# Optimization experiments

Measured on AMD Instinct MI355X. Metric: run time of the kernel, lower is better.

The kernel has to match this reference:

```python
import jax, jax.numpy as jnp
import numpy as np

N, F, H, C = 50000, 128, 4, 32  # nodes, in-features, heads, per-head dim
E = 800000
D = H * C  # concat output dim = 128


def _tconv(x, src, dst, ea, Wq, bq, Wk, bk, Wv, bv, We, Ws, bs):
    # PyG TransformerConv (concat=True, root_weight=True, beta=False, eval mode)
    n = x.shape[0]
    q = (x @ Wq + bq).reshape(n, H, C)
    k = (x @ Wk + bk).reshape(n, H, C)
    v = (x @ Wv + bv).reshape(n, H, C)
    e = (ea @ We).reshape(-1, H, C)            # edge embedding [E,H,C]
    kj = k[src] + e                            # gathered keys + edge emb
    alpha = jnp.einsum('ehc,ehc->eh', q[dst], kj) / jnp.sqrt(jnp.float32(C))
    amax = jax.ops.segment_max(alpha, dst, num_segments=n)
    ex = jnp.exp(alpha - amax[dst])
    denom = jax.ops.segment_sum(ex, dst, num_segments=n)
    w = ex / (denom[dst] + 1e-16)              # segment softmax over in-edges
    msg = (v[src] + e) * w[:, :, None]
    out = jax.ops.segment_sum(msg, dst, num_segments=n).reshape(n, D)
    return out + x @ Ws + bs                   # skip connection


def setup_inputs() -> dict:
    key = jax.random.key(0)
    ks = jax.random.split(key, 24)
    s = lambda i, shape, scale: jax.random.normal(ks[i], shape, dtype=jnp.float32) * scale
    inp = {
        'x': s(0, (N, F), 1.0),
        'edge_index': jax.random.randint(ks[1], (2, E), 0, N),
        'edge_attr': s(2, (E,), 1.0),
        # layer 1 (in = F)
        'Wq1': s(3, (F, D), 1.0 / np.sqrt(F)), 'bq1': jnp.zeros((D,), jnp.float32),
        'Wk1': s(4, (F, D), 1.0 / np.sqrt(F)), 'bk1': jnp.zeros((D,), jnp.float32),
        'Wv1': s(5, (F, D), 1.0 / np.sqrt(F)), 'bv1': jnp.zeros((D,), jnp.float32),
        'We1': s(6, (1, D), 1.0),
        'Ws1': s(7, (F, D), 1.0 / np.sqrt(F)), 'bs1': jnp.zeros((D,), jnp.float32),
        # layer 2 (in = D)
        'Wq2': s(8, (D, D), 1.0 / np.sqrt(D)), 'bq2': jnp.zeros((D,), jnp.float32),
        'Wk2': s(9, (D, D), 1.0 / np.sqrt(D)), 'bk2': jnp.zeros((D,), jnp.float32),
        'Wv2': s(10, (D, D), 1.0 / np.sqrt(D)), 'bv2': jnp.zeros((D,), jnp.float32),
        'We2': s(11, (1, D), 1.0),
        'Ws2': s(12, (D, D), 1.0 / np.sqrt(D)), 'bs2': jnp.zeros((D,), jnp.float32),
    }
    return inp


def reference(x, edge_index, edge_attr,
              Wq1, bq1, Wk1, bk1, Wv1, bv1, We1, Ws1, bs1,
              Wq2, bq2, Wk2, bk2, Wv2, bv2, We2, Ws2, bs2):
    src, dst = edge_index[0], edge_index[1]
    ea = edge_attr.reshape(-1, 1)
    h = _tconv(x, src, dst, ea, Wq1, bq1, Wk1, bk1, Wv1, bv1, We1, Ws1, bs1)
    h = jax.nn.relu(h)  # dropout is identity in eval mode
    h = _tconv(h, src, dst, ea, Wq2, bq2, Wk2, bk2, Wv2, bv2, We2, Ws2, bs2)
    return jax.nn.relu(h)
```

## Files before the change

### kernel.cpp

```cpp
#include <hip/hip_runtime.h>


#define TPB 256

typedef __attribute__((ext_vector_type(8))) short short8v;
typedef __attribute__((ext_vector_type(8))) unsigned short ushort8v;
typedef __attribute__((ext_vector_type(4))) float f32x4;

__device__ __forceinline__ unsigned short f2bf(float f) {
    unsigned u = __float_as_uint(f);
    u = (u + 0x7FFFu + ((u >> 16) & 1u)) >> 16;
    return (unsigned short)u;
}
__device__ __forceinline__ float bf2f(unsigned short s) {
    return __uint_as_float((unsigned)s << 16);
}
__device__ __forceinline__ float exp2_hw(float x) {
    float r;
    asm("v_exp_f32 %0, %1" : "=v"(r) : "v"(x));
    return r;
}

__global__ void __launch_bounds__(TPB) prepack_k(
    const float* __restrict__ Wq1, const float* __restrict__ Wk1,
    const float* __restrict__ Wv1, const float* __restrict__ Ws1,
    const float* __restrict__ Wq2, const float* __restrict__ Wk2,
    const float* __restrict__ Wv2, const float* __restrict__ Ws2,
    unsigned short* __restrict__ pack)
{
    int i = blockIdx.x * TPB + threadIdx.x;
    int j = i & 7, l = (i >> 3) & 63, t = (i >> 9) & 3, c = (i >> 11) & 7, g = (i >> 14) & 7;
    const float* Wt[8] = {Wq1, Wk1, Wv1, Ws1, Wq2, Wk2, Wv2, Ws2};
    const float* W = Wt[g];
    int kk = t * 32 + (l >> 4) * 8 + j;
    int nn = c * 16 + (l & 15);
    pack[i] = f2bf(W[kk * 128 + nn]);
}

template <bool AF32>
__global__ void __launch_bounds__(TPB) gemm_mfma_k(
    const void* __restrict__ Av, int M,
    const unsigned short* __restrict__ pack,
    const float* __restrict__ bq, const float* __restrict__ bk,
    const float* __restrict__ bv, const float* __restrict__ bs,
    unsigned short* __restrict__ oq, unsigned short* __restrict__ ok,
    unsigned short* __restrict__ ov, float* __restrict__ os)
{
    const int g = blockIdx.y;
    const int row0 = blockIdx.x * 128;
    const int wv = threadIdx.x >> 6;
    const int lane = threadIdx.x & 63;
    const int rbase = row0 + wv * 32;
    const int rlo = lane & 15;
    const int kg = (lane >> 4) * 8;
    const int rof = (lane >> 4) * 4;

    const short8v z8 = {0, 0, 0, 0, 0, 0, 0, 0};
    short8v a[2][4];
#pragma unroll
    for (int m = 0; m < 2; ++m) {
        int row = rbase + m * 16 + rlo;
        if (row >= M) {
#pragma unroll
            for (int t = 0; t < 4; ++t) a[m][t] = z8;
        } else if (AF32) {
            const float* Af = (const float*)Av + (size_t)row * 128 + kg;
#pragma unroll
            for (int t = 0; t < 4; ++t) {
                float4 lo = *(const float4*)(Af + t * 32);
                float4 hi = *(const float4*)(Af + t * 32 + 4);
                short8v p;
                p[0] = (short)f2bf(lo.x); p[1] = (short)f2bf(lo.y);
                p[2] = (short)f2bf(lo.z); p[3] = (short)f2bf(lo.w);
                p[4] = (short)f2bf(hi.x); p[5] = (short)f2bf(hi.y);
                p[6] = (short)f2bf(hi.z); p[7] = (short)f2bf(hi.w);
                a[m][t] = p;
            }
        } else {
            const unsigned short* Ab = (const unsigned short*)Av + (size_t)row * 128 + kg;
#pragma unroll
            for (int t = 0; t < 4; ++t)
                a[m][t] = *(const short8v*)(Ab + t * 32);
        }
    }

    f32x4 acc[2][8];
#pragma unroll
    for (int m = 0; m < 2; ++m)
#pragma unroll
        for (int c = 0; c < 8; ++c)
            acc[m][c] = (f32x4){0.f, 0.f, 0.f, 0.f};

    const unsigned short* bp = pack + (size_t)g * (8 * 4 * 512);
#pragma unroll
    for (int c = 0; c < 8; ++c) {
        short8v b[4];
#pragma unroll
        for (int t = 0; t < 4; ++t)
            b[t] = *(const short8v*)(bp + (c * 4 + t) * 512 + lane * 8);
#pragma unroll
        for (int t = 0; t < 4; ++t) {
            acc[0][c] = __builtin_amdgcn_mfma_f32_16x16x32_bf16(a[0][t], b[t], acc[0][c], 0, 0, 0);
            acc[1][c] = __builtin_amdgcn_mfma_f32_16x16x32_bf16(a[1][t], b[t], acc[1][c], 0, 0, 0);
        }
    }

    const float* bias = g == 0 ? bq : (g == 1 ? bk : (g == 2 ? bv : bs));
    if (g == 3) {
#pragma unroll
        for (int c = 0; c < 8; ++c) {
            float bb = bias[c * 16 + rlo];
#pragma unroll
            for (int m = 0; m < 2; ++m)
#pragma unroll
                for (int j = 0; j < 4; ++j) {
                    int row = rbase + m * 16 + rof + j;
                    if (row < M) os[(size_t)row * 128 + c * 16 + rlo] = acc[m][c][j] + bb;
                }
        }
    } else {
        unsigned short* out = g == 0 ? oq : (g == 1 ? ok : ov);
#pragma unroll
        for (int c = 0; c < 8; ++c) {
            float bb = bias[c * 16 + rlo];
#pragma unroll
            for (int m = 0; m < 2; ++m)
#pragma unroll
                for (int j = 0; j < 4; ++j) {
                    int row = rbase + m * 16 + rof + j;
                    if (row < M) out[(size_t)row * 128 + c * 16 + rlo] = f2bf(acc[m][c][j] + bb);
                }
        }
    }
}

__global__ void __launch_bounds__(TPB) hist_k(const int* __restrict__ dst,
                                              int* __restrict__ deg, int E)
{
    int e = blockIdx.x * TPB + threadIdx.x;
    if (e < E) atomicAdd(&deg[dst[e]], 1);
}

__global__ void __launch_bounds__(TPB) scan_a_k(const int* __restrict__ deg, int n,
                                                int* __restrict__ incl,
                                                int* __restrict__ bsum)
{
    __shared__ int ts[TPB];
    const int base = blockIdx.x * 1024;
    int vals[4], s = 0;
#pragma unroll
    for (int j = 0; j < 4; ++j) {
        int i = base + threadIdx.x * 4 + j;
        vals[j] = (i < n) ? deg[i] : 0;
        s += vals[j];
    }
    ts[threadIdx.x] = s;
    __syncthreads();
    for (int off = 1; off < TPB; off <<= 1) {
        int u = (threadIdx.x >= off) ? ts[threadIdx.x - off] : 0;
        __syncthreads();
        ts[threadIdx.x] += u;
        __syncthreads();
    }
    int run = ts[threadIdx.x] - s;
#pragma unroll
    for (int j = 0; j < 4; ++j) {
        run += vals[j];
        int i = base + threadIdx.x * 4 + j;
        if (i < n) incl[i] = run;
    }
    if (threadIdx.x == TPB - 1) bsum[blockIdx.x] = ts[TPB - 1];
}

__global__ void __launch_bounds__(TPB) scan_b_k(int* __restrict__ bsum, int nb)
{
    __shared__ int ts[TPB];
    int t = threadIdx.x;
    int v = (t < nb) ? bsum[t] : 0;
    ts[t] = v;
    __syncthreads();
    for (int off = 1; off < TPB; off <<= 1) {
        int u = (t >= off) ? ts[t - off] : 0;
        __syncthreads();
        ts[t] += u;
        __syncthreads();
    }
    if (t < nb) bsum[t] = ts[t] - v;
}

__global__ void __launch_bounds__(TPB) finalize_k(const int* __restrict__ incl,
                                                  const int* __restrict__ deg,
                                                  const int* __restrict__ bsum, int n,
                                                  int* __restrict__ row_ptr,
                                                  int* __restrict__ cursor)
{
    const int base = blockIdx.x * 1024;
    const int boff = bsum[blockIdx.x];
#pragma unroll
    for (int j = 0; j < 4; ++j) {
        int i = base + threadIdx.x * 4 + j;
        if (i < n) {
            int iv = incl[i] + boff;
            int st = iv - deg[i];
            row_ptr[i] = st;
            cursor[i] = st;
            if (i == n - 1) row_ptr[n] = iv;
        }
    }
}

__global__ void __launch_bounds__(TPB) scatter_k(
    const int* __restrict__ src, const int* __restrict__ dst,
    const float* __restrict__ ea, int* __restrict__ cursor,
    int2* __restrict__ csr_pair, int E)
{
    int e = blockIdx.x * TPB + threadIdx.x;
    if (e >= E) return;
    int pos = atomicAdd(&cursor[dst[e]], 1);
    csr_pair[pos] = make_int2(src[e], __float_as_int(ea[e]));
}

template <bool BF16OUT>
__global__ void __launch_bounds__(TPB) node_attn_k(
    const unsigned short* __restrict__ q, const unsigned short* __restrict__ k,
    const unsigned short* __restrict__ v, const float* __restrict__ skip,
    const float* __restrict__ We,
    const int* __restrict__ row_ptr, const int2* __restrict__ csr_pair,
    void* __restrict__ outp, int n)
{
    const int node = blockIdx.x * 16 + (threadIdx.x >> 4);
    if (node >= n) return;
    const int l16 = threadIdx.x & 15;
    const int c8 = l16 * 8;

    const float C2 = 0.17677669529663687f * 1.44269504088896f;

    float we8[8], qv[8];
    {
        float4 wlo = *(const float4*)(We + c8);
        float4 whi = *(const float4*)(We + c8 + 4);
        we8[0] = wlo.x; we8[1] = wlo.y; we8[2] = wlo.z; we8[3] = wlo.w;
        we8[4] = whi.x; we8[5] = whi.y; we8[6] = whi.z; we8[7] = whi.w;
        ushort8v qu = *(const ushort8v*)(q + (size_t)node * 128 + c8);
#pragma unroll
        for (int i = 0; i < 8; ++i) qv[i] = bf2f((unsigned short)qu[i]) * C2;
    }

    float qwe = 0.f;
#pragma unroll
    for (int i = 0; i < 8; ++i) qwe = fmaf(qv[i], we8[i], qwe);
    qwe += __shfl_xor(qwe, 1);
    qwe += __shfl_xor(qwe, 2);

    const int p0 = row_ptr[node], p1 = row_ptr[node + 1];

    float m = -3.4e38f, l = 0.f, sae = 0.f;
    float acc[8];
#pragma unroll
    for (int i = 0; i < 8; ++i) acc[i] = 0.f;

    for (int j = p0; j < p1; j += 4) {
        const int last = p1 - 1;
        int2 pr0 = csr_pair[j];
        int2 pr1 = csr_pair[min(j + 1, last)];
        int2 pr2 = csr_pair[min(j + 2, last)];
        int2 pr3 = csr_pair[min(j + 3, last)];
        ushort8v ku0 = *(const ushort8v*)(k + (unsigned)pr0.x * 128u + c8);
        ushort8v ku1 = *(const ushort8v*)(k + (unsigned)pr1.x * 128u + c8);
        ushort8v ku2 = *(const ushort8v*)(k + (unsigned)pr2.x * 128u + c8);
        ushort8v ku3 = *(const ushort8v*)(k + (unsigned)pr3.x * 128u + c8);
        ushort8v vu0 = *(const ushort8v*)(v + (unsigned)pr0.x * 128u + c8);
        ushort8v vu1 = *(const ushort8v*)(v + (unsigned)pr1.x * 128u + c8);
        ushort8v vu2 = *(const ushort8v*)(v + (unsigned)pr2.x * 128u + c8);
        ushort8v vu3 = *(const ushort8v*)(v + (unsigned)pr3.x * 128u + c8);

        float d0 = 0.f, d1 = 0.f, d2 = 0.f, d3 = 0.f;
#pragma unroll
        for (int i = 0; i < 8; ++i) {
            d0 = fmaf(bf2f((unsigned short)ku0[i]), qv[i], d0);
            d1 = fmaf(bf2f((unsigned short)ku1[i]), qv[i], d1);
            d2 = fmaf(bf2f((unsigned short)ku2[i]), qv[i], d2);
            d3 = fmaf(bf2f((unsigned short)ku3[i]), qv[i], d3);
        }
        d0 += __shfl_xor(d0, 1); d0 += __shfl_xor(d0, 2);
        d1 += __shfl_xor(d1, 1); d1 += __shfl_xor(d1, 2);
        d2 += __shfl_xor(d2, 1); d2 += __shfl_xor(d2, 2);
        d3 += __shfl_xor(d3, 1); d3 += __shfl_xor(d3, 2);

        float ea0 = __int_as_float(pr0.y), ea1 = __int_as_float(pr1.y);
        float ea2 = __int_as_float(pr2.y), ea3 = __int_as_float(pr3.y);
        float al0 = fmaf(ea0, qwe, d0);
        float al1 = (j + 1 < p1) ? fmaf(ea1, qwe, d1) : -3.4e38f;
        float al2 = (j + 2 < p1) ? fmaf(ea2, qwe, d2) : -3.4e38f;
        float al3 = (j + 3 < p1) ? fmaf(ea3, qwe, d3) : -3.4e38f;

        float mn = fmaxf(m, fmaxf(fmaxf(al0, al1), fmaxf(al2, al3)));
        float sc = exp2_hw(m - mn);
        float pe0 = exp2_hw(al0 - mn), pe1 = exp2_hw(al1 - mn);
        float pe2 = exp2_hw(al2 - mn), pe3 = exp2_hw(al3 - mn);

        l = fmaf(l, sc, (pe0 + pe1) + (pe2 + pe3));
        sae = fmaf(sae, sc, fmaf(pe3, ea3, fmaf(pe2, ea2, fmaf(pe1, ea1, pe0 * ea0))));
#pragma unroll
        for (int i = 0; i < 8; ++i) {
            float mv = fmaf(pe0, bf2f((unsigned short)vu0[i]),
                       fmaf(pe1, bf2f((unsigned short)vu1[i]),
                       fmaf(pe2, bf2f((unsigned short)vu2[i]),
                            pe3 * bf2f((unsigned short)vu3[i]))));
            acc[i] = fmaf(acc[i], sc, mv);
        }
        m = mn;
    }

    float inv = 1.f / (l + 1e-16f);
    float4 sklo = *(const float4*)(skip + (size_t)node * 128 + c8);
    float4 skhi = *(const float4*)(skip + (size_t)node * 128 + c8 + 4);
    float sk[8] = {sklo.x, sklo.y, sklo.z, sklo.w, skhi.x, skhi.y, skhi.z, skhi.w};
    float o[8];
#pragma unroll
    for (int i = 0; i < 8; ++i)
        o[i] = fmaxf(fmaf(fmaf(sae, we8[i], acc[i]), inv, sk[i]), 0.f);

    if (BF16OUT) {
        ushort8v ov;
#pragma unroll
        for (int i = 0; i < 8; ++i) ov[i] = f2bf(o[i]);
        *(ushort8v*)((unsigned short*)outp + (size_t)node * 128 + c8) = ov;
    } else {
        float* op = (float*)outp + (size_t)node * 128 + c8;
        *(float4*)op = make_float4(o[0], o[1], o[2], o[3]);
        *(float4*)(op + 4) = make_float4(o[4], o[5], o[6], o[7]);
    }
}

extern "C" void kernel_launch(void* const* d_in, const int* in_sizes, int n_in,
                              void* d_out, int out_size, void* d_ws, size_t ws_size,
                              hipStream_t stream)
{
    const float* x   = (const float*)d_in[0];
    const int*   ei  = (const int*)d_in[1];
    const float* ea  = (const float*)d_in[2];
    const float* Wq1 = (const float*)d_in[3];  const float* bq1 = (const float*)d_in[4];
    const float* Wk1 = (const float*)d_in[5];  const float* bk1 = (const float*)d_in[6];
    const float* Wv1 = (const float*)d_in[7];  const float* bv1 = (const float*)d_in[8];
    const float* We1 = (const float*)d_in[9];
    const float* Ws1 = (const float*)d_in[10]; const float* bs1 = (const float*)d_in[11];
    const float* Wq2 = (const float*)d_in[12]; const float* bq2 = (const float*)d_in[13];
    const float* Wk2 = (const float*)d_in[14]; const float* bk2 = (const float*)d_in[15];
    const float* Wv2 = (const float*)d_in[16]; const float* bv2 = (const float*)d_in[17];
    const float* We2 = (const float*)d_in[18];
    const float* Ws2 = (const float*)d_in[19]; const float* bs2 = (const float*)d_in[20];

    const int N = in_sizes[0] / 128;
    const int E = in_sizes[1] / 2;
    const int* src = ei;
    const int* dst = ei + E;
    float* outf = (float*)d_out;

    unsigned short* q  = (unsigned short*)d_ws;
    unsigned short* k  = q + (size_t)N * 128;
    unsigned short* v  = k + (size_t)N * 128;
    float*          s  = (float*)(v + (size_t)N * 128);
    unsigned short* xb = (unsigned short*)(s + (size_t)N * 128);
    unsigned short* pk = xb + (size_t)N * 128;
    int*   row_ptr = (int*)(pk + 131072);
    int*   deg     = row_ptr + (N + 1);
    int*   incl    = deg + N;
    int*   cursor  = incl + N;
    int*   bsum    = cursor + N;
    int2*  csr_pair = (int2*)(((uintptr_t)(bsum + 256) + 7) & ~(uintptr_t)7);

    const int gE   = (E + TPB - 1) / TPB;
    const int nb   = (N + 1023) / 1024;
    const int gN16 = (N + 15) / 16;
    const int gG   = (N + 127) / 128;
    const dim3 gGd(gG, 4);

    hipMemsetAsync(deg, 0, (size_t)N * sizeof(int), stream);
    hist_k<<<gE, TPB, 0, stream>>>(dst, deg, E);
    scan_a_k<<<nb, TPB, 0, stream>>>(deg, N, incl, bsum);
    scan_b_k<<<1, TPB, 0, stream>>>(bsum, nb);
    finalize_k<<<nb, TPB, 0, stream>>>(incl, deg, bsum, N, row_ptr, cursor);
    scatter_k<<<gE, TPB, 0, stream>>>(src, dst, ea, cursor, csr_pair, E);

    prepack_k<<<131072 / TPB, TPB, 0, stream>>>(Wq1, Wk1, Wv1, Ws1,
                                                Wq2, Wk2, Wv2, Ws2, pk);

    gemm_mfma_k<true><<<gGd, TPB, 0, stream>>>(x, N, pk, bq1, bk1, bv1, bs1,
                                               q, k, v, s);
    node_attn_k<true><<<gN16, TPB, 0, stream>>>(q, k, v, s, We1, row_ptr, csr_pair,
                                                xb, N);
    gemm_mfma_k<false><<<gGd, TPB, 0, stream>>>(xb, N, pk + 65536, bq2, bk2, bv2, bs2,
                                                q, k, v, s);
    node_attn_k<false><<<gN16, TPB, 0, stream>>>(q, k, v, s, We2, row_ptr, csr_pair,
                                                 outf, N);
}
```

Before: 312.8 us.

## Software-pipeline neighbor gathers in attention and pre-convert input to bf16

The attention kernel now double-buffers its edge loop: while one batch of four edges is being processed, it issues the CSR pair loads and the K/V row gathers for the following batches, so memory latency overlaps with compute. Separately, the fp32 input is converted to bf16 once by a new kernel, so the first GEMM no longer converts x in each of its four column-group blocks and reads half the bytes. In exchange the attention kernel holds more registers for the two stages, which may lower occupancy, and there is one extra launch plus an extra pass over x.

```diff
diff --git a/kernel.cpp b/kernel.cpp
--- a/kernel.cpp
+++ b/kernel.cpp
@@ -19,6 +19,18 @@
     float r;
     asm("v_exp_f32 %0, %1" : "=v"(r) : "v"(x));
     return r;
+}
+
+__global__ void __launch_bounds__(TPB) cvt_bf16_k(const float* __restrict__ in,
+                                                  unsigned short* __restrict__ out,
+                                                  int n4)
+{
+    int i = blockIdx.x * TPB + threadIdx.x;
+    if (i >= n4) return;
+    float4 v = *(const float4*)(in + (size_t)i * 4);
+    ushort4 o;
+    o.x = f2bf(v.x); o.y = f2bf(v.y); o.z = f2bf(v.z); o.w = f2bf(v.w);
+    *(ushort4*)(out + (size_t)i * 4) = o;
 }
 
 __global__ void __launch_bounds__(TPB) prepack_k(
@@ -37,9 +49,8 @@
     pack[i] = f2bf(W[kk * 128 + nn]);
 }
 
-template <bool AF32>
 __global__ void __launch_bounds__(TPB) gemm_mfma_k(
-    const void* __restrict__ Av, int M,
+    const unsigned short* __restrict__ A, int M,
     const unsigned short* __restrict__ pack,
     const float* __restrict__ bq, const float* __restrict__ bk,
     const float* __restrict__ bv, const float* __restrict__ bs,
@@ -60,28 +71,10 @@
 #pragma unroll
     for (int m = 0; m < 2; ++m) {
         int row = rbase + m * 16 + rlo;
-        if (row >= M) {
-#pragma unroll
-            for (int t = 0; t < 4; ++t) a[m][t] = z8;
-        } else if (AF32) {
-            const float* Af = (const float*)Av + (size_t)row * 128 + kg;
-#pragma unroll
-            for (int t = 0; t < 4; ++t) {
-                float4 lo = *(const float4*)(Af + t * 32);
-                float4 hi = *(const float4*)(Af + t * 32 + 4);
-                short8v p;
-                p[0] = (short)f2bf(lo.x); p[1] = (short)f2bf(lo.y);
-                p[2] = (short)f2bf(lo.z); p[3] = (short)f2bf(lo.w);
-                p[4] = (short)f2bf(hi.x); p[5] = (short)f2bf(hi.y);
-                p[6] = (short)f2bf(hi.z); p[7] = (short)f2bf(hi.w);
-                a[m][t] = p;
-            }
-        } else {
-            const unsigned short* Ab = (const unsigned short*)Av + (size_t)row * 128 + kg;
-#pragma unroll
-            for (int t = 0; t < 4; ++t)
-                a[m][t] = *(const short8v*)(Ab + t * 32);
-        }
+#pragma unroll
+        for (int t = 0; t < 4; ++t)
+            a[m][t] = (row < M) ? *(const short8v*)(A + (size_t)row * 128 + t * 32 + kg)
+                                : z8;
     }
 
     f32x4 acc[2][8];
@@ -220,6 +213,65 @@
     csr_pair[pos] = make_int2(src[e], __float_as_int(ea[e]));
 }
 
+struct Stage {
+    int2 p[4];
+    ushort8v ku[4], vu[4];
+};
+
+__device__ __forceinline__ void attn_step(
+    Stage& cur, Stage& nxt, int j, int p1, int last,
+    const int2* __restrict__ csr_pair,
+    const unsigned short* __restrict__ k, const unsigned short* __restrict__ v,
+    int c8, const float* qv, float qwe,
+    float& m, float& l, float& sae, float* acc)
+{
+    float ea0 = __int_as_float(cur.p[0].y), ea1 = __int_as_float(cur.p[1].y);
+    float ea2 = __int_as_float(cur.p[2].y), ea3 = __int_as_float(cur.p[3].y);
+#pragma unroll
+    for (int t = 0; t < 4; ++t) cur.p[t] = csr_pair[min(j + 8 + t, last)];
+
+#pragma unroll
+    for (int t = 0; t < 4; ++t) {
+        nxt.ku[t] = *(const ushort8v*)(k + (unsigned)nxt.p[t].x * 128u + c8);
+        nxt.vu[t] = *(const ushort8v*)(v + (unsigned)nxt.p[t].x * 128u + c8);
+    }
+
+    float d0 = 0.f, d1 = 0.f, d2 = 0.f, d3 = 0.f;
+#pragma unroll
+    for (int i = 0; i < 8; ++i) {
+        d0 = fmaf(bf2f((unsigned short)cur.ku[0][i]), qv[i], d0);
+        d1 = fmaf(bf2f((unsigned short)cur.ku[1][i]), qv[i], d1);
+        d2 = fmaf(bf2f((unsigned short)cur.ku[2][i]), qv[i], d2);
+        d3 = fmaf(bf2f((unsigned short)cur.ku[3][i]), qv[i], d3);
+    }
+    d0 += __shfl_xor(d0, 1); d0 += __shfl_xor(d0, 2);
+    d1 += __shfl_xor(d1, 1); d1 += __shfl_xor(d1, 2);
+    d2 += __shfl_xor(d2, 1); d2 += __shfl_xor(d2, 2);
+    d3 += __shfl_xor(d3, 1); d3 += __shfl_xor(d3, 2);
+
+    float al0 = fmaf(ea0, qwe, d0);
+    float al1 = (j + 1 < p1) ? fmaf(ea1, qwe, d1) : -3.4e38f;
+    float al2 = (j + 2 < p1) ? fmaf(ea2, qwe, d2) : -3.4e38f;
+    float al3 = (j + 3 < p1) ? fmaf(ea3, qwe, d3) : -3.4e38f;
+
+    float mn = fmaxf(m, fmaxf(fmaxf(al0, al1), fmaxf(al2, al3)));
+    float sc = exp2_hw(m - mn);
+    float pe0 = exp2_hw(al0 - mn), pe1 = exp2_hw(al1 - mn);
+    float pe2 = exp2_hw(al2 - mn), pe3 = exp2_hw(al3 - mn);
+
+    l = fmaf(l, sc, (pe0 + pe1) + (pe2 + pe3));
+    sae = fmaf(sae, sc, fmaf(pe3, ea3, fmaf(pe2, ea2, fmaf(pe1, ea1, pe0 * ea0))));
+#pragma unroll
+    for (int i = 0; i < 8; ++i) {
+        float mv = fmaf(pe0, bf2f((unsigned short)cur.vu[0][i]),
+                   fmaf(pe1, bf2f((unsigned short)cur.vu[1][i]),
+                   fmaf(pe2, bf2f((unsigned short)cur.vu[2][i]),
+                        pe3 * bf2f((unsigned short)cur.vu[3][i]))));
+        acc[i] = fmaf(acc[i], sc, mv);
+    }
+    m = mn;
+}
+
 template <bool BF16OUT>
 __global__ void __launch_bounds__(TPB) node_attn_k(
     const unsigned short* __restrict__ q, const unsigned short* __restrict__ k,
@@ -235,22 +287,19 @@
 
     const float C2 = 0.17677669529663687f * 1.44269504088896f;
 
-    float we8[8], qv[8];
+    float qv[8];
+    float qwe;
     {
         float4 wlo = *(const float4*)(We + c8);
         float4 whi = *(const float4*)(We + c8 + 4);
-        we8[0] = wlo.x; we8[1] = wlo.y; we8[2] = wlo.z; we8[3] = wlo.w;
-        we8[4] = whi.x; we8[5] = whi.y; we8[6] = whi.z; we8[7] = whi.w;
         ushort8v qu = *(const ushort8v*)(q + (size_t)node * 128 + c8);
 #pragma unroll
         for (int i = 0; i < 8; ++i) qv[i] = bf2f((unsigned short)qu[i]) * C2;
-    }
-
-    float qwe = 0.f;
-#pragma unroll
-    for (int i = 0; i < 8; ++i) qwe = fmaf(qv[i], we8[i], qwe);
-    qwe += __shfl_xor(qwe, 1);
-    qwe += __shfl_xor(qwe, 2);
+        qwe = qv[0] * wlo.x + qv[1] * wlo.y + qv[2] * wlo.z + qv[3] * wlo.w +
+              qv[4] * whi.x + qv[5] * whi.y + qv[6] * whi.z + qv[7] * whi.w;
+        qwe += __shfl_xor(qwe, 1);
+        qwe += __shfl_xor(qwe, 2);
+    }
 
     const int p0 = row_ptr[node], p1 = row_ptr[node + 1];
 
@@ -259,60 +308,31 @@
 #pragma unroll
     for (int i = 0; i < 8; ++i) acc[i] = 0.f;
 
-    for (int j = p0; j < p1; j += 4) {
+    if (p0 < p1) {
         const int last = p1 - 1;
-        int2 pr0 = csr_pair[j];
-        int2 pr1 = csr_pair[min(j + 1, last)];
-        int2 pr2 = csr_pair[min(j + 2, last)];
-        int2 pr3 = csr_pair[min(j + 3, last)];
-        ushort8v ku0 = *(const ushort8v*)(k + (unsigned)pr0.x * 128u + c8);
-        ushort8v ku1 = *(const ushort8v*)(k + (unsigned)pr1.x * 128u + c8);
-        ushort8v ku2 = *(const ushort8v*)(k + (unsigned)pr2.x * 128u + c8);
-        ushort8v ku3 = *(const ushort8v*)(k + (unsigned)pr3.x * 128u + c8);
-        ushort8v vu0 = *(const ushort8v*)(v + (unsigned)pr0.x * 128u + c8);
-        ushort8v vu1 = *(const ushort8v*)(v + (unsigned)pr1.x * 128u + c8);
-        ushort8v vu2 = *(const ushort8v*)(v + (unsigned)pr2.x * 128u + c8);
-        ushort8v vu3 = *(const ushort8v*)(v + (unsigned)pr3.x * 128u + c8);
-
-        float d0 = 0.f, d1 = 0.f, d2 = 0.f, d3 = 0.f;
-#pragma unroll
-        for (int i = 0; i < 8; ++i) {
-            d0 = fmaf(bf2f((unsigned short)ku0[i]), qv[i], d0);
-            d1 = fmaf(bf2f((unsigned short)ku1[i]), qv[i], d1);
-            d2 = fmaf(bf2f((unsigned short)ku2[i]), qv[i], d2);
-            d3 = fmaf(bf2f((unsigned short)ku3[i]), qv[i], d3);
-        }
-        d0 += __shfl_xor(d0, 1); d0 += __shfl_xor(d0, 2);
-        d1 += __shfl_xor(d1, 1); d1 += __shfl_xor(d1, 2);
-        d2 += __shfl_xor(d2, 1); d2 += __shfl_xor(d2, 2);
-        d3 += __shfl_xor(d3, 1); d3 += __shfl_xor(d3, 2);
-
-        float ea0 = __int_as_float(pr0.y), ea1 = __int_as_float(pr1.y);
-        float ea2 = __int_as_float(pr2.y), ea3 = __int_as_float(pr3.y);
-        float al0 = fmaf(ea0, qwe, d0);
-        float al1 = (j + 1 < p1) ? fmaf(ea1, qwe, d1) : -3.4e38f;
-        float al2 = (j + 2 < p1) ? fmaf(ea2, qwe, d2) : -3.4e38f;
-        float al3 = (j + 3 < p1) ? fmaf(ea3, qwe, d3) : -3.4e38f;
-
-        float mn = fmaxf(m, fmaxf(fmaxf(al0, al1), fmaxf(al2, al3)));
-        float sc = exp2_hw(m - mn);
-        float pe0 = exp2_hw(al0 - mn), pe1 = exp2_hw(al1 - mn);
-        float pe2 = exp2_hw(al2 - mn), pe3 = exp2_hw(al3 - mn);
-
-        l = fmaf(l, sc, (pe0 + pe1) + (pe2 + pe3));
-        sae = fmaf(sae, sc, fmaf(pe3, ea3, fmaf(pe2, ea2, fmaf(pe1, ea1, pe0 * ea0))));
-#pragma unroll
-        for (int i = 0; i < 8; ++i) {
-            float mv = fmaf(pe0, bf2f((unsigned short)vu0[i]),
-                       fmaf(pe1, bf2f((unsigned short)vu1[i]),
-                       fmaf(pe2, bf2f((unsigned short)vu2[i]),
-                            pe3 * bf2f((unsigned short)vu3[i]))));
-            acc[i] = fmaf(acc[i], sc, mv);
-        }
-        m = mn;
+        Stage A, B;
+#pragma unroll
+        for (int t = 0; t < 4; ++t) A.p[t] = csr_pair[min(p0 + t, last)];
+#pragma unroll
+        for (int t = 0; t < 4; ++t) B.p[t] = csr_pair[min(p0 + 4 + t, last)];
+#pragma unroll
+        for (int t = 0; t < 4; ++t) {
+            A.ku[t] = *(const ushort8v*)(k + (unsigned)A.p[t].x * 128u + c8);
+            A.vu[t] = *(const ushort8v*)(v + (unsigned)A.p[t].x * 128u + c8);
+        }
+        int j = p0;
+        for (;;) {
+            attn_step(A, B, j, p1, last, csr_pair, k, v, c8, qv, qwe, m, l, sae, acc);
+            j += 4; if (j >= p1) break;
+            attn_step(B, A, j, p1, last, csr_pair, k, v, c8, qv, qwe, m, l, sae, acc);
+            j += 4; if (j >= p1) break;
+        }
     }
 
     float inv = 1.f / (l + 1e-16f);
+    float4 wlo = *(const float4*)(We + c8);
+    float4 whi = *(const float4*)(We + c8 + 4);
+    float we8[8] = {wlo.x, wlo.y, wlo.z, wlo.w, whi.x, whi.y, whi.z, whi.w};
     float4 sklo = *(const float4*)(skip + (size_t)node * 128 + c8);
     float4 skhi = *(const float4*)(skip + (size_t)node * 128 + c8 + 4);
     float sk[8] = {sklo.x, sklo.y, sklo.z, sklo.w, skhi.x, skhi.y, skhi.z, skhi.w};
@@ -373,6 +393,7 @@
     const int gE   = (E + TPB - 1) / TPB;
     const int nb   = (N + 1023) / 1024;
     const int gN16 = (N + 15) / 16;
+    const int gCv  = (N * 128 / 4 + TPB - 1) / TPB;
     const int gG   = (N + 127) / 128;
     const dim3 gGd(gG, 4);
 
@@ -385,13 +406,13 @@
 
     prepack_k<<<131072 / TPB, TPB, 0, stream>>>(Wq1, Wk1, Wv1, Ws1,
                                                 Wq2, Wk2, Wv2, Ws2, pk);
-
-    gemm_mfma_k<true><<<gGd, TPB, 0, stream>>>(x, N, pk, bq1, bk1, bv1, bs1,
-                                               q, k, v, s);
+    cvt_bf16_k<<<gCv, TPB, 0, stream>>>(x, xb, N * 128 / 4);
+
+    gemm_mfma_k<<<gGd, TPB, 0, stream>>>(xb, N, pk, bq1, bk1, bv1, bs1, q, k, v, s);
     node_attn_k<true><<<gN16, TPB, 0, stream>>>(q, k, v, s, We1, row_ptr, csr_pair,
                                                 xb, N);
-    gemm_mfma_k<false><<<gGd, TPB, 0, stream>>>(xb, N, pk + 65536, bq2, bk2, bv2, bs2,
-                                                q, k, v, s);
+    gemm_mfma_k<<<gGd, TPB, 0, stream>>>(xb, N, pk + 65536, bq2, bk2, bv2, bs2,
+                                         q, k, v, s);
     node_attn_k<false><<<gN16, TPB, 0, stream>>>(q, k, v, s, We2, row_ptr, csr_pair,
                                                  outf, N);
 }
```

Result: no change. 311.3 us (-0.5%).

## Interleave K and V rows, switch GEMM to 32x32 MFMA, pre-convert x to bf16

Applied to the files above, without the earlier changes.

K and V projections are now stored interleaved in a single buffer with 256-element rows, so each gathered source node's key and value sit next to each other in memory. The GEMM moves from 16x16x32 to 32x32x16 bf16 MFMA tiles, and the weight prepack layout changes to match. Layer-1 input x is converted to bf16 by an extra section of the prepack kernel, which removes the templated fp32 A-load path from the GEMM. The gather is meant to get better locality, at the cost of an extra pass over x and a different accumulator and register footprint in the GEMM.

```diff
diff --git a/kernel.cpp b/kernel.cpp
--- a/kernel.cpp
+++ b/kernel.cpp
@@ -5,7 +5,7 @@
 
 typedef __attribute__((ext_vector_type(8))) short short8v;
 typedef __attribute__((ext_vector_type(8))) unsigned short ushort8v;
-typedef __attribute__((ext_vector_type(4))) float f32x4;
+typedef __attribute__((ext_vector_type(16))) float f32x16;
 
 __device__ __forceinline__ unsigned short f2bf(float f) {
     unsigned u = __float_as_uint(f);
@@ -21,115 +21,101 @@
     return r;
 }
 
-__global__ void __launch_bounds__(TPB) prepack_k(
+__global__ void __launch_bounds__(TPB) prep_cvt_k(
     const float* __restrict__ Wq1, const float* __restrict__ Wk1,
     const float* __restrict__ Wv1, const float* __restrict__ Ws1,
     const float* __restrict__ Wq2, const float* __restrict__ Wk2,
     const float* __restrict__ Wv2, const float* __restrict__ Ws2,
-    unsigned short* __restrict__ pack)
-{
-    int i = blockIdx.x * TPB + threadIdx.x;
-    int j = i & 7, l = (i >> 3) & 63, t = (i >> 9) & 3, c = (i >> 11) & 7, g = (i >> 14) & 7;
-    const float* Wt[8] = {Wq1, Wk1, Wv1, Ws1, Wq2, Wk2, Wv2, Ws2};
-    const float* W = Wt[g];
-    int kk = t * 32 + (l >> 4) * 8 + j;
-    int nn = c * 16 + (l & 15);
-    pack[i] = f2bf(W[kk * 128 + nn]);
-}
-
-template <bool AF32>
+    unsigned short* __restrict__ pack,
+    const float* __restrict__ x, unsigned short* __restrict__ xb, int n4)
+{
+    if (blockIdx.x < 512) {
+        int i = blockIdx.x * TPB + threadIdx.x;
+        int j = i & 7, lane = (i >> 3) & 63, t = (i >> 9) & 7, nc = (i >> 12) & 3, g = (i >> 14) & 7;
+        const float* Wt[8] = {Wq1, Wk1, Wv1, Ws1, Wq2, Wk2, Wv2, Ws2};
+        const float* W = Wt[g];
+        int kk = t * 16 + (lane >> 5) * 8 + j;
+        int nn = nc * 32 + (lane & 31);
+        pack[i] = f2bf(W[kk * 128 + nn]);
+    } else {
+        int i = (blockIdx.x - 512) * TPB + threadIdx.x;
+        if (i >= n4) return;
+        float4 v = *(const float4*)(x + (size_t)i * 4);
+        ushort4 o;
+        o.x = f2bf(v.x); o.y = f2bf(v.y); o.z = f2bf(v.z); o.w = f2bf(v.w);
+        *(ushort4*)(xb + (size_t)i * 4) = o;
+    }
+}
+
 __global__ void __launch_bounds__(TPB) gemm_mfma_k(
-    const void* __restrict__ Av, int M,
+    const unsigned short* __restrict__ A, int M,
     const unsigned short* __restrict__ pack,
     const float* __restrict__ bq, const float* __restrict__ bk,
     const float* __restrict__ bv, const float* __restrict__ bs,
-    unsigned short* __restrict__ oq, unsigned short* __restrict__ ok,
-    unsigned short* __restrict__ ov, float* __restrict__ os)
+    unsigned short* __restrict__ oq, unsigned short* __restrict__ okv,
+    float* __restrict__ os)
 {
     const int g = blockIdx.y;
     const int row0 = blockIdx.x * 128;
     const int wv = threadIdx.x >> 6;
     const int lane = threadIdx.x & 63;
     const int rbase = row0 + wv * 32;
-    const int rlo = lane & 15;
-    const int kg = (lane >> 4) * 8;
-    const int rof = (lane >> 4) * 4;
+    const int arow = rbase + (lane & 31);
+    const int kh = (lane >> 5) * 8;
 
     const short8v z8 = {0, 0, 0, 0, 0, 0, 0, 0};
-    short8v a[2][4];
-#pragma unroll
-    for (int m = 0; m < 2; ++m) {
-        int row = rbase + m * 16 + rlo;
-        if (row >= M) {
-#pragma unroll
-            for (int t = 0; t < 4; ++t) a[m][t] = z8;
-        } else if (AF32) {
-            const float* Af = (const float*)Av + (size_t)row * 128 + kg;
-#pragma unroll
-            for (int t = 0; t < 4; ++t) {
-                float4 lo = *(const float4*)(Af + t * 32);
-                float4 hi = *(const float4*)(Af + t * 32 + 4);
-                short8v p;
-                p[0] = (short)f2bf(lo.x); p[1] = (short)f2bf(lo.y);
-                p[2] = (short)f2bf(lo.z); p[3] = (short)f2bf(lo.w);
-                p[4] = (short)f2bf(hi.x); p[5] = (short)f2bf(hi.y);
-                p[6] = (short)f2bf(hi.z); p[7] = (short)f2bf(hi.w);
-                a[m][t] = p;
+    short8v a[8];
+    if (arow < M) {
+        const unsigned short* Ap = A + (size_t)arow * 128 + kh;
+#pragma unroll
+        for (int t = 0; t < 8; ++t) a[t] = *(const short8v*)(Ap + t * 16);
+    } else {
+#pragma unroll
+        for (int t = 0; t < 8; ++t) a[t] = z8;
+    }
+
+    f32x16 acc[4];
+#pragma unroll
+    for (int nc = 0; nc < 4; ++nc)
+#pragma unroll
+        for (int r = 0; r < 16; ++r) acc[nc][r] = 0.f;
+
+    const unsigned short* bp = pack + (size_t)g * 16384;
+#pragma unroll
+    for (int nc = 0; nc < 4; ++nc) {
+#pragma unroll
+        for (int t = 0; t < 8; ++t) {
+            short8v b = *(const short8v*)(bp + (nc * 8 + t) * 512 + lane * 8);
+            acc[nc] = __builtin_amdgcn_mfma_f32_32x32x16_bf16(a[t], b, acc[nc], 0, 0, 0);
+        }
+    }
+
+    const float* bias = g == 0 ? bq : (g == 1 ? bk : (g == 2 ? bv : bs));
+    const int col = lane & 31;
+    const int rb2 = rbase + 4 * (lane >> 5);
+    if (g == 3) {
+#pragma unroll
+        for (int nc = 0; nc < 4; ++nc) {
+            float bb = bias[nc * 32 + col];
+#pragma unroll
+            for (int r = 0; r < 16; ++r) {
+                int row = rb2 + (r & 3) + 8 * (r >> 2);
+                if (row < M) os[(size_t)row * 128 + nc * 32 + col] = acc[nc][r] + bb;
             }
-        } else {
-            const unsigned short* Ab = (const unsigned short*)Av + (size_t)row * 128 + kg;
-#pragma unroll
-            for (int t = 0; t < 4; ++t)
-                a[m][t] = *(const short8v*)(Ab + t * 32);
-        }
-    }
-
-    f32x4 acc[2][8];
-#pragma unroll
-    for (int m = 0; m < 2; ++m)
-#pragma unroll
-        for (int c = 0; c < 8; ++c)
-            acc[m][c] = (f32x4){0.f, 0.f, 0.f, 0.f};
-
-    const unsigned short* bp = pack + (size_t)g * (8 * 4 * 512);
-#pragma unroll
-    for (int c = 0; c < 8; ++c) {
-        short8v b[4];
-#pragma unroll
-        for (int t = 0; t < 4; ++t)
-            b[t] = *(const short8v*)(bp + (c * 4 + t) * 512 + lane * 8);
-#pragma unroll
-        for (int t = 0; t < 4; ++t) {
-            acc[0][c] = __builtin_amdgcn_mfma_f32_16x16x32_bf16(a[0][t], b[t], acc[0][c], 0, 0, 0);
-            acc[1][c] = __builtin_amdgcn_mfma_f32_16x16x32_bf16(a[1][t], b[t], acc[1][c], 0, 0, 0);
-        }
-    }
-
-    const float* bias = g == 0 ? bq : (g == 1 ? bk : (g == 2 ? bv : bs));
-    if (g == 3) {
-#pragma unroll
-        for (int c = 0; c < 8; ++c) {
-            float bb = bias[c * 16 + rlo];
-#pragma unroll
-            for (int m = 0; m < 2; ++m)
-#pragma unroll
-                for (int j = 0; j < 4; ++j) {
-                    int row = rbase + m * 16 + rof + j;
-                    if (row < M) os[(size_t)row * 128 + c * 16 + rlo] = acc[m][c][j] + bb;
-                }
         }
     } else {
-        unsigned short* out = g == 0 ? oq : (g == 1 ? ok : ov);
-#pragma unroll
-        for (int c = 0; c < 8; ++c) {
-            float bb = bias[c * 16 + rlo];
-#pragma unroll
-            for (int m = 0; m < 2; ++m)
-#pragma unroll
-                for (int j = 0; j < 4; ++j) {
-                    int row = rbase + m * 16 + rof + j;
-                    if (row < M) out[(size_t)row * 128 + c * 16 + rlo] = f2bf(acc[m][c][j] + bb);
-                }
+        unsigned short* out = g == 0 ? oq : okv;
+        const int stride = g == 0 ? 128 : 256;
+        const int goff = g == 2 ? 128 : 0;
+#pragma unroll
+        for (int nc = 0; nc < 4; ++nc) {
+            float bb = bias[nc * 32 + col];
+#pragma unroll
+            for (int r = 0; r < 16; ++r) {
+                int row = rb2 + (r & 3) + 8 * (r >> 2);
+                if (row < M)
+                    out[(size_t)row * stride + goff + nc * 32 + col] = f2bf(acc[nc][r] + bb);
+            }
         }
     }
 }
@@ -222,9 +208,8 @@
 
 template <bool BF16OUT>
 __global__ void __launch_bounds__(TPB) node_attn_k(
-    const unsigned short* __restrict__ q, const unsigned short* __restrict__ k,
-    const unsigned short* __restrict__ v, const float* __restrict__ skip,
-    const float* __restrict__ We,
+    const unsigned short* __restrict__ q, const unsigned short* __restrict__ kv,
+    const float* __restrict__ skip, const float* __restrict__ We,
     const int* __restrict__ row_ptr, const int2* __restrict__ csr_pair,
     void* __restrict__ outp, int n)
 {
@@ -265,14 +250,18 @@
         int2 pr1 = csr_pair[min(j + 1, last)];
         int2 pr2 = csr_pair[min(j + 2, last)];
         int2 pr3 = csr_pair[min(j + 3, last)];
-        ushort8v ku0 = *(const ushort8v*)(k + (unsigned)pr0.x * 128u + c8);
-        ushort8v ku1 = *(const ushort8v*)(k + (unsigned)pr1.x * 128u + c8);
-        ushort8v ku2 = *(const ushort8v*)(k + (unsigned)pr2.x * 128u + c8);
-        ushort8v ku3 = *(const ushort8v*)(k + (unsigned)pr3.x * 128u + c8);
-        ushort8v vu0 = *(const ushort8v*)(v + (unsigned)pr0.x * 128u + c8);
-        ushort8v vu1 = *(const ushort8v*)(v + (unsigned)pr1.x * 128u + c8);
-        ushort8v vu2 = *(const ushort8v*)(v + (unsigned)pr2.x * 128u + c8);
-        ushort8v vu3 = *(const ushort8v*)(v + (unsigned)pr3.x * 128u + c8);
+        const unsigned short* b0 = kv + (unsigned)pr0.x * 256u + c8;
+        const unsigned short* b1 = kv + (unsigned)pr1.x * 256u + c8;
+        const unsigned short* b2 = kv + (unsigned)pr2.x * 256u + c8;
+        const unsigned short* b3 = kv + (unsigned)pr3.x * 256u + c8;
+        ushort8v ku0 = *(const ushort8v*)b0;
+        ushort8v ku1 = *(const ushort8v*)b1;
+        ushort8v ku2 = *(const ushort8v*)b2;
+        ushort8v ku3 = *(const ushort8v*)b3;
+        ushort8v vu0 = *(const ushort8v*)(b0 + 128);
+        ushort8v vu1 = *(const ushort8v*)(b1 + 128);
+        ushort8v vu2 = *(const ushort8v*)(b2 + 128);
+        ushort8v vu3 = *(const ushort8v*)(b3 + 128);
 
         float d0 = 0.f, d1 = 0.f, d2 = 0.f, d3 = 0.f;
 #pragma unroll
@@ -358,9 +347,8 @@
     float* outf = (float*)d_out;
 
     unsigned short* q  = (unsigned short*)d_ws;
-    unsigned short* k  = q + (size_t)N * 128;
-    unsigned short* v  = k + (size_t)N * 128;
-    float*          s  = (float*)(v + (size_t)N * 128);
+    unsigned short* kv = q + (size_t)N * 128;
+    float*          s  = (float*)(kv + (size_t)N * 256);
     unsigned short* xb = (unsigned short*)(s + (size_t)N * 128);
     unsigned short* pk = xb + (size_t)N * 128;
     int*   row_ptr = (int*)(pk + 131072);
@@ -373,6 +361,8 @@
     const int gE   = (E + TPB - 1) / TPB;
     const int nb   = (N + 1023) / 1024;
     const int gN16 = (N + 15) / 16;
+    const int n4   = N * 128 / 4;
+    const int gPC  = 512 + (n4 + TPB - 1) / TPB;
     const int gG   = (N + 127) / 128;
     const dim3 gGd(gG, 4);
 
@@ -383,15 +373,14 @@
     finalize_k<<<nb, TPB, 0, stream>>>(incl, deg, bsum, N, row_ptr, cursor);
     scatter_k<<<gE, TPB, 0, stream>>>(src, dst, ea, cursor, csr_pair, E);
 
-    prepack_k<<<131072 / TPB, TPB, 0, stream>>>(Wq1, Wk1, Wv1, Ws1,
-                                                Wq2, Wk2, Wv2, Ws2, pk);
-
-    gemm_mfma_k<true><<<gGd, TPB, 0, stream>>>(x, N, pk, bq1, bk1, bv1, bs1,
-                                               q, k, v, s);
-    node_attn_k<true><<<gN16, TPB, 0, stream>>>(q, k, v, s, We1, row_ptr, csr_pair,
+    prep_cvt_k<<<gPC, TPB, 0, stream>>>(Wq1, Wk1, Wv1, Ws1, Wq2, Wk2, Wv2, Ws2,
+                                        pk, x, xb, n4);
+
+    gemm_mfma_k<<<gGd, TPB, 0, stream>>>(xb, N, pk, bq1, bk1, bv1, bs1, q, kv, s);
+    node_attn_k<true><<<gN16, TPB, 0, stream>>>(q, kv, s, We1, row_ptr, csr_pair,
                                                 xb, N);
-    gemm_mfma_k<false><<<gGd, TPB, 0, stream>>>(xb, N, pk + 65536, bq2, bk2, bv2, bs2,
-                                                q, k, v, s);
-    node_attn_k<false><<<gN16, TPB, 0, stream>>>(q, k, v, s, We2, row_ptr, csr_pair,
+    gemm_mfma_k<<<gGd, TPB, 0, stream>>>(xb, N, pk + 65536, bq2, bk2, bv2, bs2,
+                                         q, kv, s);
+    node_attn_k<false><<<gN16, TPB, 0, stream>>>(q, kv, s, We2, row_ptr, csr_pair,
                                                  outf, N);
 }
```

New measurement: 324.2 us. 3.6% more time.
